# Kernel optimization log

Hardware: AMD Instinct MI355X
Metric: run time of the kernel (lower is better)

The kernel has to match this reference:

```python
import jax, jax.numpy as jnp
import numpy as np

D_MODEL = 1024
N_HEADS = 16
D_HEAD = D_MODEL // N_HEADS


def setup_inputs() -> dict:
    key = jax.random.key(0)
    ks = jax.random.split(key, 5)
    scale = 1.0 / np.sqrt(D_MODEL)
    return {
        "x": jax.random.normal(ks[0], (2, 2048, D_MODEL), dtype=jnp.float32),
        "W_q": jax.random.normal(ks[1], (D_MODEL, D_MODEL), dtype=jnp.float32) * scale,
        "W_k": jax.random.normal(ks[2], (D_MODEL, D_MODEL), dtype=jnp.float32) * scale,
        "W_v": jax.random.normal(ks[3], (D_MODEL, D_MODEL), dtype=jnp.float32) * scale,
        "W_o": jax.random.normal(ks[4], (D_MODEL, D_MODEL), dtype=jnp.float32) * scale,
    }


def reference(x, W_q, W_k, W_v, W_o):
    B, S, _ = x.shape
    # nn.Linear computes x @ W.T; weights stored [out, in]
    def proj(W):
        y = jnp.einsum("bsd,ed->bse", x, W)
        return y.reshape(B, S, N_HEADS, D_HEAD).transpose(0, 2, 1, 3)  # [B,H,S,Dh]

    q, k, v = proj(W_q), proj(W_k), proj(W_v)
    scores = jnp.einsum("bhqd,bhkd->bhqk", q, k) / jnp.sqrt(jnp.float32(D_HEAD))
    causal = jnp.triu(jnp.ones((S, S), dtype=bool), k=1)
    scores = jnp.where(causal, -jnp.inf, scores)
    attn = jax.nn.softmax(scores, axis=-1)
    out = jnp.einsum("bhqk,bhkd->bhqd", attn, v)  # [B,H,S,Dh]
    out = out.transpose(0, 2, 1, 3).reshape(B, S, D_MODEL)
    return jnp.einsum("bsd,ed->bse", out, W_o)
```

## Files before the change

kernel.cpp:

```cpp
#include <hip/hip_runtime.h>


#define DMODEL 1024
#define NHEADS 16
#define DHEAD  64
#define SEQ    2048
#define BATCH  2
#define MROWS  (BATCH * SEQ)

typedef __bf16 bf16x8 __attribute__((ext_vector_type(8)));
typedef __bf16 bf16x4 __attribute__((ext_vector_type(4)));
typedef float  f32x4  __attribute__((ext_vector_type(4)));

__device__ __forceinline__ f32x4 mfma16(bf16x8 a, bf16x8 b, f32x4 c) {
    return __builtin_amdgcn_mfma_f32_16x16x32_bf16(a, b, c, 0, 0, 0);
}

__device__ __forceinline__ bf16x8 ld8(const float* p) {
    const f32x4 a0 = *(const f32x4*)p;
    const f32x4 a1 = *(const f32x4*)(p + 4);
    bf16x8 v;
    v[0] = (__bf16)a0[0]; v[1] = (__bf16)a0[1];
    v[2] = (__bf16)a0[2]; v[3] = (__bf16)a0[3];
    v[4] = (__bf16)a1[0]; v[5] = (__bf16)a1[1];
    v[6] = (__bf16)a1[2]; v[7] = (__bf16)a1[3];
    return v;
}

__device__ __forceinline__ void gll16(const __bf16* g, __bf16* l) {
    __builtin_amdgcn_global_load_lds(
        (const __attribute__((address_space(1))) void*)g,
        (__attribute__((address_space(3))) void*)l,
        16, 0, 0);
}

__global__ __launch_bounds__(256) void cvt_kernel(const float* __restrict__ x,
                                                  const float* __restrict__ Wq,
                                                  const float* __restrict__ Wk,
                                                  const float* __restrict__ Wv,
                                                  const float* __restrict__ Wo,
                                                  __bf16* __restrict__ xb,
                                                  __bf16* __restrict__ wcat) {
    const int c = blockIdx.x * 256 + threadIdx.x;
    if (c < 524288) {
        *(bf16x8*)(xb + (size_t)c * 8) = ld8(x + (size_t)c * 8);
    } else {
        const int i = c - 524288;
        const int w = i >> 17;
        const int j = i & 131071;
        const float* src = (w == 0) ? Wq : (w == 1) ? Wk : (w == 2) ? Wv : Wo;
        *(bf16x8*)(wcat + (size_t)w * DMODEL * DMODEL + (size_t)j * 8) =
            ld8(src + (size_t)j * 8);
    }
}

template <typename TC, int MI>
__device__ __forceinline__ void gemm_bb_body(const __bf16* __restrict__ A,
                                             const __bf16* __restrict__ W,
                                             TC* __restrict__ C,
                                             __bf16* __restrict__ VT,
                                             bool vt, int m0, int bn0, int cn0,
                                             float scale) {
    constexpr int K = DMODEL;
    constexpr int TM = MI * 32;
    __shared__ __align__(16) __bf16 As[2][TM][32];
    __shared__ __align__(16) __bf16 Bs[2][128][32];

    const int tid  = threadIdx.x;
    const int lane = tid & 63;
    const int wave = tid >> 6;
    const int quad = lane >> 4;
    const int l16  = lane & 15;
    const int wm   = wave & 1;
    const int wn   = wave >> 1;

    const int srow = lane >> 2;
    const int scol = (lane & 3) * 8;

    const __bf16* a0p = A + (size_t)(m0 + wave * 16 + srow) * K + scol;
    const __bf16* a1p = A + (size_t)(m0 + 64 + wave * 16 + srow) * K + scol;
    const __bf16* b0p = W + (size_t)(bn0 + wave * 16 + srow) * K + scol;
    const __bf16* b1p = W + (size_t)(bn0 + 64 + wave * 16 + srow) * K + scol;

    f32x4 acc[MI][4] = {};

    gll16(a0p, &As[0][wave * 16][0]);
    if (MI == 4) gll16(a1p, &As[0][64 + wave * 16][0]);
    gll16(b0p, &Bs[0][wave * 16][0]);
    gll16(b1p, &Bs[0][64 + wave * 16][0]);
    __syncthreads();

    int cur = 0;
    for (int k0 = 0; k0 < K; k0 += 32) {
        if (k0 + 32 < K) {
            const int kn = k0 + 32;
            gll16(a0p + kn, &As[cur ^ 1][wave * 16][0]);
            if (MI == 4) gll16(a1p + kn, &As[cur ^ 1][64 + wave * 16][0]);
            gll16(b0p + kn, &Bs[cur ^ 1][wave * 16][0]);
            gll16(b1p + kn, &Bs[cur ^ 1][64 + wave * 16][0]);
        }

        bf16x8 af[MI], bfr[4];
#pragma unroll
        for (int i = 0; i < MI; ++i)
            af[i] = *(const bf16x8*)(&As[cur][wm * (MI * 16) + i * 16 + l16][quad * 8]);
#pragma unroll
        for (int j = 0; j < 4; ++j)
            bfr[j] = *(const bf16x8*)(&Bs[cur][wn * 64 + j * 16 + l16][quad * 8]);
#pragma unroll
        for (int mi = 0; mi < MI; ++mi)
#pragma unroll
            for (int ni = 0; ni < 4; ++ni)
                acc[mi][ni] = mfma16(af[mi], bfr[ni], acc[mi][ni]);

        __syncthreads();
        cur ^= 1;
    }

    if (!vt) {
#pragma unroll
        for (int mi = 0; mi < MI; ++mi)
#pragma unroll
            for (int ni = 0; ni < 4; ++ni)
#pragma unroll
                for (int r = 0; r < 4; ++r) {
                    int row = m0 + wm * (MI * 16) + mi * 16 + quad * 4 + r;
                    int col = cn0 + wn * 64 + ni * 16 + l16;
                    C[(size_t)row * DMODEL + col] = (TC)(acc[mi][ni][r] * scale);
                }
    } else {
#pragma unroll
        for (int mi = 0; mi < MI; ++mi)
#pragma unroll
            for (int ni = 0; ni < 4; ++ni) {
                const int m  = m0 + wm * (MI * 16) + mi * 16 + quad * 4;
                const int hd = cn0 + wn * 64 + ni * 16 + l16;
                bf16x4 v4;
#pragma unroll
                for (int r = 0; r < 4; ++r) v4[r] = (__bf16)acc[mi][ni][r];
                *(bf16x4*)(VT + (size_t)hd * MROWS + m) = v4;
            }
    }
}

#define QSCALE 0.1803368801111204f

__global__ __launch_bounds__(256) void qkv_kernel(const __bf16* __restrict__ X,
                                                  const __bf16* __restrict__ wcat,
                                                  __bf16* __restrict__ Q,
                                                  __bf16* __restrict__ K,
                                                  __bf16* __restrict__ VT) {
    const int bn0 = blockIdx.x * 128;
    const int z   = bn0 >> 10;
    const int cn0 = bn0 - (z << 10);
    __bf16* Y = (z == 0) ? Q : K;
    const float scale = (z == 0) ? QSCALE : 1.0f;
    gemm_bb_body<__bf16, 4>(X, wcat, Y, VT, z == 2,
                            blockIdx.y * 128, bn0, cn0, scale);
}

__global__ __launch_bounds__(256) void out_gemm_kernel(const __bf16* __restrict__ A,
                                                       const __bf16* __restrict__ W,
                                                       float* __restrict__ C) {
    gemm_bb_body<float, 2>(A, W, C, nullptr, false,
                           blockIdx.y * 64, blockIdx.x * 128, blockIdx.x * 128,
                           1.0f);
}

__global__ __launch_bounds__(256) void attn_kernel(const __bf16* __restrict__ Q,
                                                   const __bf16* __restrict__ Kg,
                                                   const __bf16* __restrict__ VTg,
                                                   __bf16* __restrict__ O) {
    const int bh  = blockIdx.x;
    const int y   = blockIdx.y;
    const int ya  = y >> 3, yr = y & 7;
    const int qt2 = (ya == 0) ? (31 - yr)
                  : (ya == 1) ? (16 + yr)
                  : (ya == 2) ? (15 - yr)
                  :             yr;
    const int b = bh >> 4, h = bh & 15;
    const size_t base = (size_t)b * SEQ * DMODEL + (size_t)h * DHEAD;

    const int tid  = threadIdx.x;
    const int lane = tid & 63;
    const int wave = tid >> 6;
    const int quad = lane >> 4;
    const int l16  = lane & 15;

    __shared__ __align__(16) __bf16 Ks[64][64];
    __shared__ __align__(16) __bf16 Vs[64][64];
    __shared__ __align__(16) __bf16 Ps[4][2][16][40];

    const int sr = lane >> 3;
    const int sc = ((lane & 7) ^ sr) * 8;

    const int qrow = qt2 * 64 + wave * 16 + l16;

    const bf16x8 qf0 = *(const bf16x8*)(Q + base + (size_t)qrow * DMODEL + quad * 8);
    const bf16x8 qf1 = *(const bf16x8*)(Q + base + (size_t)qrow * DMODEL + 32 + quad * 8);

    const __bf16* kp = Kg + base + (size_t)(wave * 16 + sr) * DMODEL + sc;
    const __bf16* vp = VTg + (size_t)(h * 64 + wave * 16 + sr) * MROWS
                           + (size_t)b * SEQ + sc;

    bf16x8 ones;
#pragma unroll
    for (int i = 0; i < 8; ++i) ones[i] = (__bf16)1.0f;

    f32x4 oacc[4] = {};
    f32x4 lacc = {};

    const int ntiles = qt2 + 1;
    const int gsw = (l16 & 7);

    for (int kt = 0; kt < ntiles; ++kt) {
        const int k0 = kt * 64;
        __syncthreads();
        {
            const __bf16* kpt = kp + (size_t)k0 * DMODEL;
            const __bf16* vpt = vp + k0;
            gll16(kpt, &Ks[wave * 16][0]);
            gll16(kpt + (size_t)8 * DMODEL, &Ks[wave * 16 + 8][0]);
            gll16(vpt, &Vs[wave * 16][0]);
            gll16(vpt + (size_t)8 * MROWS, &Vs[wave * 16 + 8][0]);
        }
        __syncthreads();

        const bool diag = (kt == ntiles - 1);

        f32x4 s[4];
#pragma unroll
        for (int g = 0; g < 4; ++g) {
            const bf16x8 kfa = *(const bf16x8*)(&Ks[g * 16 + l16][(quad ^ gsw) * 8]);
            const bf16x8 kfb = *(const bf16x8*)(&Ks[g * 16 + l16][((quad + 4) ^ gsw) * 8]);
            f32x4 t = {};
            t = mfma16(kfa, qf0, t);
            t = mfma16(kfb, qf1, t);
            s[g] = t;
        }

        bf16x4 w4[4];
        if (!diag) {
#pragma unroll
            for (int g = 0; g < 4; ++g)
#pragma unroll
                for (int r = 0; r < 4; ++r)
                    w4[g][r] = (__bf16)exp2f(s[g][r]);
        } else {
#pragma unroll
            for (int g = 0; g < 4; ++g)
#pragma unroll
                for (int r = 0; r < 4; ++r) {
                    const int kk = k0 + g * 16 + quad * 4 + r;
                    w4[g][r] = (kk <= qrow) ? (__bf16)exp2f(s[g][r]) : (__bf16)0.f;
                }
        }

#pragma unroll
        for (int g = 0; g < 4; ++g)
            *(bf16x4*)(&Ps[wave][g >> 1][l16][(g & 1) * 16 + quad * 4]) = w4[g];

        const bf16x8 pf0 = *(const bf16x8*)(&Ps[wave][0][l16][quad * 8]);
        const bf16x8 pf1 = *(const bf16x8*)(&Ps[wave][1][l16][quad * 8]);
        lacc = mfma16(ones, pf0, lacc);
        lacc = mfma16(ones, pf1, lacc);
#pragma unroll
        for (int f = 0; f < 4; ++f) {
            const bf16x8 vfa = *(const bf16x8*)(&Vs[f * 16 + l16][(quad ^ gsw) * 8]);
            const bf16x8 vfb = *(const bf16x8*)(&Vs[f * 16 + l16][((quad + 4) ^ gsw) * 8]);
            f32x4 t = oacc[f];
            t = mfma16(vfa, pf0, t);
            t = mfma16(vfb, pf1, t);
            oacc[f] = t;
        }
    }

    const float l_i = lacc[0];
    const float inv = (l_i > 0.f) ? (1.f / l_i) : 0.f;
#pragma unroll
    for (int f = 0; f < 4; ++f) {
        bf16x4 o;
#pragma unroll
        for (int r = 0; r < 4; ++r) o[r] = (__bf16)(oacc[f][r] * inv);
        *(bf16x4*)(O + base + (size_t)qrow * DMODEL + f * 16 + quad * 4) = o;
    }
}

extern "C" void kernel_launch(void* const* d_in, const int* in_sizes, int n_in,
                              void* d_out, int out_size, void* d_ws, size_t ws_size,
                              hipStream_t stream) {
    const float* x  = (const float*)d_in[0];
    const float* Wq = (const float*)d_in[1];
    const float* Wk = (const float*)d_in[2];
    const float* Wv = (const float*)d_in[3];
    const float* Wo = (const float*)d_in[4];
    float* out = (float*)d_out;

    const size_t tm = (size_t)MROWS * DMODEL;
    const size_t tw = (size_t)DMODEL * DMODEL;
    __bf16* Q    = (__bf16*)d_ws;
    __bf16* K    = Q + tm;
    __bf16* VT   = K + tm;
    __bf16* xb   = VT + tm;
    __bf16* wcat = xb + tm;

    cvt_kernel<<<4096, 256, 0, stream>>>(x, Wq, Wk, Wv, Wo, xb, wcat);

    dim3 g1(3072 / 128, MROWS / 128);
    qkv_kernel<<<g1, 256, 0, stream>>>(xb, wcat, Q, K, VT);

    dim3 g2(BATCH * NHEADS, SEQ / 64);
    attn_kernel<<<g2, 256, 0, stream>>>(Q, K, VT, Q);

    dim3 g3(DMODEL / 128, MROWS / 64);
    out_gemm_kernel<<<g3, 256, 0, stream>>>(Q, wcat + 3 * tw, out);
}
```

Before: 181.2 us.

## Double-buffer K tiles in LDS and load V fragments directly into registers

The attention loop now double-buffers the K tile in shared memory, issuing the next tile's async global-to-LDS load before computing on the current one. The per-iteration barrier count drops from two to one. V^T fragments are read straight from global memory into registers at the start of each iteration instead of being staged through shared memory. This aims to hide K load latency and cut LDS traffic, at the cost of more registers and uncoalesced per-lane V reads that every wave repeats.

Result: slower. 216.0 us (+19.2%).

```diff
diff --git a/kernel.cpp b/kernel.cpp
--- a/kernel.cpp
+++ b/kernel.cpp
@@ -187,8 +187,7 @@
     const int quad = lane >> 4;
     const int l16  = lane & 15;
 
-    __shared__ __align__(16) __bf16 Ks[64][64];
-    __shared__ __align__(16) __bf16 Vs[64][64];
+    __shared__ __align__(16) __bf16 Ks[2][64][64];
     __shared__ __align__(16) __bf16 Ps[4][2][16][40];
 
     const int sr = lane >> 3;
@@ -200,8 +199,8 @@
     const bf16x8 qf1 = *(const bf16x8*)(Q + base + (size_t)qrow * DMODEL + 32 + quad * 8);
 
     const __bf16* kp = Kg + base + (size_t)(wave * 16 + sr) * DMODEL + sc;
-    const __bf16* vp = VTg + (size_t)(h * 64 + wave * 16 + sr) * MROWS
-                           + (size_t)b * SEQ + sc;
+    const __bf16* vb = VTg + (size_t)(h * 64 + l16) * MROWS
+                           + (size_t)b * SEQ + quad * 8;
 
     bf16x8 ones;
 #pragma unroll
@@ -213,26 +212,35 @@
     const int ntiles = qt2 + 1;
     const int gsw = (l16 & 7);
 
+    gll16(kp, &Ks[0][wave * 16][0]);
+    gll16(kp + (size_t)8 * DMODEL, &Ks[0][wave * 16 + 8][0]);
+    __syncthreads();
+
+    int cur = 0;
     for (int kt = 0; kt < ntiles; ++kt) {
         const int k0 = kt * 64;
-        __syncthreads();
-        {
-            const __bf16* kpt = kp + (size_t)k0 * DMODEL;
-            const __bf16* vpt = vp + k0;
-            gll16(kpt, &Ks[wave * 16][0]);
-            gll16(kpt + (size_t)8 * DMODEL, &Ks[wave * 16 + 8][0]);
-            gll16(vpt, &Vs[wave * 16][0]);
-            gll16(vpt + (size_t)8 * MROWS, &Vs[wave * 16 + 8][0]);
-        }
-        __syncthreads();
+
+        bf16x8 vfa[4], vfb[4];
+#pragma unroll
+        for (int f = 0; f < 4; ++f) {
+            const __bf16* vf = vb + (size_t)(f * 16) * MROWS + k0;
+            vfa[f] = *(const bf16x8*)(vf);
+            vfb[f] = *(const bf16x8*)(vf + 32);
+        }
+
+        if (kt + 1 < ntiles) {
+            const __bf16* kpt = kp + (size_t)(k0 + 64) * DMODEL;
+            gll16(kpt, &Ks[cur ^ 1][wave * 16][0]);
+            gll16(kpt + (size_t)8 * DMODEL, &Ks[cur ^ 1][wave * 16 + 8][0]);
+        }
 
         const bool diag = (kt == ntiles - 1);
 
         f32x4 s[4];
 #pragma unroll
         for (int g = 0; g < 4; ++g) {
-            const bf16x8 kfa = *(const bf16x8*)(&Ks[g * 16 + l16][(quad ^ gsw) * 8]);
-            const bf16x8 kfb = *(const bf16x8*)(&Ks[g * 16 + l16][((quad + 4) ^ gsw) * 8]);
+            const bf16x8 kfa = *(const bf16x8*)(&Ks[cur][g * 16 + l16][(quad ^ gsw) * 8]);
+            const bf16x8 kfb = *(const bf16x8*)(&Ks[cur][g * 16 + l16][((quad + 4) ^ gsw) * 8]);
             f32x4 t = {};
             t = mfma16(kfa, qf0, t);
             t = mfma16(kfb, qf1, t);
@@ -266,13 +274,14 @@
         lacc = mfma16(ones, pf1, lacc);
 #pragma unroll
         for (int f = 0; f < 4; ++f) {
-            const bf16x8 vfa = *(const bf16x8*)(&Vs[f * 16 + l16][(quad ^ gsw) * 8]);
-            const bf16x8 vfb = *(const bf16x8*)(&Vs[f * 16 + l16][((quad + 4) ^ gsw) * 8]);
             f32x4 t = oacc[f];
-            t = mfma16(vfa, pf0, t);
-            t = mfma16(vfb, pf1, t);
+            t = mfma16(vfa[f], pf0, t);
+            t = mfma16(vfb[f], pf1, t);
             oacc[f] = t;
         }
+
+        __syncthreads();
+        cur ^= 1;
     }
 
     const float l_i = lacc[0];
```
